# Optimization experiments

Hardware: AMD Instinct MI355X
Metric: run time of the kernel (lower is better)

## Reference

```python
import jax, jax.numpy as jnp
import numpy as np

V, E, H, B, T, O = 50000, 512, 1024, 128, 512, 10


def setup_inputs() -> dict:
    key = jax.random.key(0)
    ks = jax.random.split(key, 12)
    inputs = jax.random.randint(ks[0], (B, T), 0, V)  # token ids
    emb = jax.random.normal(ks[1], (V, E), jnp.float32) * 0.02

    def w(k, shape):
        # stand-in for orthogonal init: scaled gaussian, same shapes/math
        return jax.random.normal(k, shape, jnp.float32) / np.sqrt(shape[0])

    return dict(
        inputs=inputs, emb=emb,
        W_xi=w(ks[2], (E, H)), W_hi=w(ks[3], (H, H)), b_i=jnp.zeros(H, jnp.float32),
        W_xf=w(ks[4], (E, H)), W_hf=w(ks[5], (H, H)), b_f=jnp.ones(H, jnp.float32),
        W_xo=w(ks[6], (E, H)), W_ho=w(ks[7], (H, H)), b_o=jnp.zeros(H, jnp.float32),
        W_xc=w(ks[8], (E, H)), W_hc=w(ks[9], (H, H)), b_c=jnp.zeros(H, jnp.float32),
        W_hq=w(ks[10], (H, O)), b_q=jnp.zeros(O, jnp.float32),
    )


def reference(inputs, emb, W_xi, W_hi, b_i, W_xf, W_hf, b_f,
              W_xo, W_ho, b_o, W_xc, W_hc, b_c, W_hq, b_q):
    x = emb[inputs]  # [B, T, E] embedding lookup
    # Fuse the 4 input projections into one GEMM over the whole sequence
    # (same math as 4 per-step mms: sigmoid/tanh applied per-gate below).
    Wx = jnp.concatenate([W_xi, W_xf, W_xo, W_xc], axis=1)  # [E, 4H]
    Wh = jnp.concatenate([W_hi, W_hf, W_ho, W_hc], axis=1)  # [H, 4H]
    bg = jnp.concatenate([b_i, b_f, b_o, b_c])              # [4H]
    xproj = jnp.einsum('bte,eg->tbg', x, Wx) + bg           # [T, B, 4H]

    hdim = W_hi.shape[0]
    h0 = jnp.zeros((inputs.shape[0], hdim), x.dtype)

    def step(carry, xp):
        h, c = carry
        g = xp + h @ Wh                       # [B, 4H]
        i, f, o, c_tilda = jnp.split(g, 4, axis=-1)
        c = jax.nn.sigmoid(f) * c + jax.nn.sigmoid(i) * jnp.tanh(c_tilda)
        h = jax.nn.sigmoid(o) * jnp.tanh(c)
        return (h, c), None

    (h, _), _ = jax.lax.scan(step, (h0, h0), xproj)
    return jax.nn.softmax(h @ W_hq + b_q, axis=1)  # [B, 10]
```

## Files before the change

kernel.cpp:

```cpp
#include <hip/hip_runtime.h>
#include <hip/hip_fp16.h>

#define V_ 50000
#define E_ 512
#define H_ 1024
#define B_ 128
#define T_ 512
#define NG 4096

typedef _Float16 half8 __attribute__((ext_vector_type(8)));
typedef float f32x4 __attribute__((ext_vector_type(4)));

static constexpr size_t WX_OFF   = 0;
static constexpr size_t WH_OFF   = (size_t)4 << 20;
static constexpr size_t BG_OFF   = (size_t)12 << 20;
static constexpr size_t HBUF_OFF = ((size_t)12 << 20) + ((size_t)64 << 10);
static constexpr size_t BAR_OFF  = ((size_t)12 << 20) + ((size_t)640 << 10);
static constexpr size_t XF_OFF   = (size_t)16 << 20;
static constexpr size_t WS_NEED  = XF_OFF + (size_t)T_ * B_ * E_ * 2;

__device__ __forceinline__ float fsigm(float x) { return 1.f / (1.f + __expf(-x)); }
__device__ __forceinline__ float ftanh(float x) {
  float cx = fminf(fmaxf(x, -15.f), 15.f);
  float e = __expf(2.f * cx);
  return (e - 1.f) / (e + 1.f);
}
__device__ __forceinline__ half8 as_h8(f32x4 x) {
  union { f32x4 f; half8 h; } u; u.f = x; return u.h;
}

__global__ void k_diag(float* __restrict__ out, int n, unsigned wsmb) {
  int i = blockIdx.x * 256 + threadIdx.x;
  if (i < n) out[i] = (i == 0) ? (float)wsmb : 0.1f;
}

__global__ __launch_bounds__(256) void k_prep(
    const float* __restrict__ Wxi, const float* __restrict__ Wxf,
    const float* __restrict__ Wxo, const float* __restrict__ Wxc,
    const float* __restrict__ Whi, const float* __restrict__ Whf,
    const float* __restrict__ Who, const float* __restrict__ Whc,
    const float* __restrict__ bi, const float* __restrict__ bfp,
    const float* __restrict__ bo, const float* __restrict__ bc,
    char* __restrict__ ws) {
  half8* wx = (half8*)(ws + WX_OFF);
  half8* wh = (half8*)(ws + WH_OFF);
  float* bg = (float*)(ws + BG_OFF);
  half8* hb = (half8*)(ws + HBUF_OFF);
  unsigned* bar = (unsigned*)(ws + BAR_OFF);
  const float* WxA[4] = {Wxi, Wxf, Wxo, Wxc};
  const float* WhA[4] = {Whi, Whf, Who, Whc};
  const float* bA[4]  = {bi, bfp, bo, bc};

  const int ZWX = 256 * 16 * 64;
  const int ZWH = 32 * 8 * 32 * 64;
  const int ZBG = NG;
  const int ZHB = 2 * B_ * H_ / 8;
  const int ZBAR = 8 * 128 * 16 + 8 * 64 * 16 + 8 * 32 * 16 + 8 * 16;
  const int total = ZWX + ZWH + ZBG + ZHB + ZBAR;

  for (int it = blockIdx.x * 256 + threadIdx.x; it < total; it += gridDim.x * 256) {
    int i = it;
    if (i < ZWX) {
      int L = i & 63, kt = (i >> 6) & 15, ntg = i >> 10;
      int gate = ntg >> 6;
      int col = ((ntg & 63) << 4) + (L & 15);
      int k0 = (kt << 5) + ((L >> 4) << 3);
      const float* src = WxA[gate] + (size_t)k0 * H_ + col;
      half8 v;
#pragma unroll
      for (int j = 0; j < 8; j++) v[j] = (_Float16)src[(size_t)j * H_];
      wx[i] = v;
    } else if ((i -= ZWX) < ZWH) {
      int L = i & 63, kt = (i >> 6) & 31, nt = (i >> 11) & 7, hbk = i >> 14;
      int ct = nt & 1, g = nt >> 1;
      int col = (hbk << 5) + (ct << 4) + (L & 15);
      int k0 = (kt << 5) + ((L >> 4) << 3);
      const float* src = WhA[g] + (size_t)k0 * H_ + col;
      half8 v;
#pragma unroll
      for (int j = 0; j < 8; j++) v[j] = (_Float16)src[(size_t)j * H_];
      wh[i] = v;
    } else if ((i -= ZWH) < ZBG) {
      bg[i] = bA[i >> 10][i & 1023];
    } else if ((i -= ZBG) < ZHB) {
      half8 z = {};
      hb[i] = z;
    } else {
      i -= ZHB;
      bar[i] = 0u;
    }
  }
}

__global__ __launch_bounds__(256) void k_embed(const int* __restrict__ ids,
                                               const float* __restrict__ emb,
                                               char* __restrict__ ws) {
  half8* xf = (half8*)(ws + XF_OFF);
  const int t = blockIdx.x;
  for (int p = threadIdx.x; p < 128 * 64; p += 256) {
    int b = p >> 6, c8 = p & 63;
    int id = ids[b * T_ + t];
    const float* er = emb + (size_t)id * E_ + (c8 << 3);
    float4 f0 = *(const float4*)er;
    float4 f1 = *(const float4*)(er + 4);
    half8 v;
    v[0] = (_Float16)f0.x; v[1] = (_Float16)f0.y; v[2] = (_Float16)f0.z; v[3] = (_Float16)f0.w;
    v[4] = (_Float16)f1.x; v[5] = (_Float16)f1.y; v[6] = (_Float16)f1.z; v[7] = (_Float16)f1.w;
    int g = b >> 4, row = b & 15;
    xf[((size_t)(t * 8 + g) * 16 + (c8 >> 2)) * 64 + (row | ((c8 & 3) << 4))] = v;
  }
}

__global__ __launch_bounds__(256, 1) void k_lstm(char* __restrict__ ws) {
  __shared__ f32x4 red[4][8][64];
  __shared__ _Float16 hstage2[2][16][16];
  __shared__ unsigned red_ep[4];
  __shared__ int wok[4];
  __shared__ unsigned sslot, sbal;
  const half8* whf = (const half8*)(ws + WH_OFF);
  const half8* wxg = (const half8*)(ws + WX_OFF);
  const float* bgp = (const float*)(ws + BG_OFF);
  _Float16* hbuf = (_Float16*)(ws + HBUF_OFF);
  const half8* xff = (const half8*)(ws + XF_OFF);
  unsigned* bar = (unsigned*)(ws + BAR_OFF);

  const int wg = blockIdx.x;
  const int tid = threadIdx.x;
  const int L = tid & 63, w = tid >> 6;
  const int lo = L & 15, quad = L >> 4;
  unsigned* ctrp = bar + 28672;

  unsigned myxid;
  asm volatile("s_getreg_b32 %0, hwreg(HW_REG_XCC_ID)" : "=s"(myxid));
  myxid &= 7u;
  if (tid == 0)
    sslot = __hip_atomic_fetch_add(&ctrp[myxid * 16], 1u, __ATOMIC_RELAXED,
                                   __HIP_MEMORY_SCOPE_AGENT);
  __syncthreads();
  const unsigned slot = __builtin_amdgcn_readfirstlane(sslot);
  if (tid == 0) {
    unsigned cnt[8];
    while (true) {
      unsigned s = 0;
#pragma unroll
      for (int x = 0; x < 8; x++) {
        cnt[x] = __hip_atomic_load(&ctrp[x * 16], __ATOMIC_RELAXED, __HIP_MEMORY_SCOPE_AGENT);
        s += cnt[x];
      }
      if (s == 256u) break;
      __builtin_amdgcn_s_sleep(4);
    }
    unsigned ok = 1u;
#pragma unroll
    for (int x = 0; x < 8; x++) ok &= (cnt[x] == 32u) ? 1u : 0u;
    sbal = ok;
  }
  __syncthreads();
  const bool balanced = sbal != 0u;
  const int group = balanced ? (int)myxid : (wg & 7);
  const int hblk  = balanced ? (int)slot  : (wg >> 3);
  const int hbase = hblk << 5;
  unsigned* flags = bar + group * 2048;
  unsigned* probe = bar + 16384 + group * 1024;
  unsigned* votes = bar + 24576 + group * 512;

  if (balanced && w < 2 && L == 0) {
    unsigned one = 1u;
    unsigned* pp = &probe[((hblk << 1) + w) << 4];
    asm volatile("global_store_dword %0, %1, off" :: "v"(pp), "v"(one) : "memory");
  }

  half8 bw[8][8];
#pragma unroll
  for (int nt = 0; nt < 8; nt++)
#pragma unroll
    for (int k8 = 0; k8 < 8; k8++)
      bw[nt][k8] = whf[((size_t)(hblk * 8 + nt) * 32 + w * 8 + k8) * 64 + L];
  half8 wxr[8][4];
#pragma unroll
  for (int nt = 0; nt < 8; nt++)
#pragma unroll
    for (int kx = 0; kx < 4; kx++)
      wxr[nt][kx] =
          wxg[(size_t)(((nt >> 1) * 64 + (hblk << 1) + (nt & 1)) * 16 + w * 4 + kx) * 64 + L];

  bool fast = false;
  if (balanced) {
    int okw = 0;
    for (int it = 0; it < 1500 && !okw; ++it) {
      unsigned v = 1u;
      if (L < 16) {
        const unsigned* pp = &probe[(w * 16 + L) << 4];
        unsigned vv;
        asm volatile("global_load_dword %0, %1, off sc0 nt\n\ts_waitcnt vmcnt(0)"
                     : "=v"(vv) : "v"(pp) : "memory");
        v = vv;
      }
      okw = __all((int)(v != 0u));
      if (!okw) __builtin_amdgcn_s_sleep(2);
    }
    if (L == 0) wok[w] = okw;
    __syncthreads();
    const int allok = wok[0] & wok[1] & wok[2] & wok[3];
    if (tid == 0)
      __hip_atomic_store(&votes[hblk << 4], (unsigned)(allok ? 2 : 1),
                         __ATOMIC_RELAXED, __HIP_MEMORY_SCOPE_AGENT);
    unsigned fastu;
    while (true) {
      unsigned v = 2u;
      if (L < 32)
        v = __hip_atomic_load(&votes[L << 4], __ATOMIC_RELAXED, __HIP_MEMORY_SCOPE_AGENT);
      if (__all((int)(v != 0u))) { fastu = (unsigned)__all((int)(v == 2u)); break; }
      __builtin_amdgcn_s_sleep(8);
    }
    fast = fastu != 0;
  }

  const int ct = w & 1, rh = w >> 1;
  float bgr[4] = {};
#pragma unroll
  for (int g = 0; g < 4; g++) bgr[g] = bgp[g * H_ + hbase + (ct << 4) + lo];
  f32x4 cst = {};
  float cst2[2] = {};
  if (tid < 4) red_ep[tid] = 0u;

  half8 ax[4];
  {
    const half8* xb = xff + (size_t)group * (16 * 64);
#pragma unroll
    for (int kx = 0; kx < 4; kx++) ax[kx] = xb[(w * 4 + kx) * 64 + L];
  }
  __syncthreads();

  if (fast) {
    for (int t = 0; t < T_; t++) {
      const _Float16* hb = hbuf + (size_t)(t & 1) * (B_ * H_);
      _Float16* hw = hbuf + (size_t)((t + 1) & 1) * (B_ * H_);

      f32x4 ahf[8];
      const _Float16* hbp =
          hb + (((size_t)group * 32 + (size_t)(w * 8)) << 9) + ((size_t)L << 3);
      const _Float16* hbp2 = hbp + ((size_t)4 << 9);
      asm volatile("global_load_dwordx4 %0, %1, off sc0 nt"             : "=v"(ahf[0]) : "v"(hbp));
      asm volatile("global_load_dwordx4 %0, %1, off offset:1024 sc0 nt" : "=v"(ahf[1]) : "v"(hbp));
      asm volatile("global_load_dwordx4 %0, %1, off offset:2048 sc0 nt" : "=v"(ahf[2]) : "v"(hbp));
      asm volatile("global_load_dwordx4 %0, %1, off offset:3072 sc0 nt" : "=v"(ahf[3]) : "v"(hbp));
      asm volatile("global_load_dwordx4 %0, %1, off sc0 nt"             : "=v"(ahf[4]) : "v"(hbp2));
      asm volatile("global_load_dwordx4 %0, %1, off offset:1024 sc0 nt" : "=v"(ahf[5]) : "v"(hbp2));
      asm volatile("global_load_dwordx4 %0, %1, off offset:2048 sc0 nt" : "=v"(ahf[6]) : "v"(hbp2));
      asm volatile("global_load_dwordx4 %0, %1, off offset:3072 sc0 nt" : "=v"(ahf[7]) : "v"(hbp2));
      asm volatile("s_waitcnt vmcnt(0)" ::: "memory");
      __builtin_amdgcn_sched_barrier(0);

      f32x4 acc[8] = {};
#pragma unroll
      for (int kx = 0; kx < 4; kx++)
#pragma unroll
        for (int nt = 0; nt < 8; nt++)
          acc[nt] = __builtin_amdgcn_mfma_f32_16x16x32_f16(ax[kx], wxr[nt][kx], acc[nt], 0, 0, 0);
#pragma unroll
      for (int k8 = 0; k8 < 8; k8++)
#pragma unroll
        for (int nt = 0; nt < 8; nt++)
          acc[nt] = __builtin_amdgcn_mfma_f32_16x16x32_f16(as_h8(ahf[k8]), bw[nt][k8], acc[nt], 0, 0, 0);
#pragma unroll
      for (int nt = 0; nt < 8; nt++) red[w][nt][L] = acc[nt];
      __syncthreads();

      {
        float ga[4], gb[4];
#pragma unroll
        for (int g = 0; g < 4; g++) {
          f32x4 s = red[0][g * 2 + ct][L];
          s += red[1][g * 2 + ct][L];
          s += red[2][g * 2 + ct][L];
          s += red[3][g * 2 + ct][L];
          ga[g] = rh ? s[2] : s[0];
          gb[g] = rh ? s[3] : s[1];
        }
        if (L == 0)
          __hip_atomic_store(&red_ep[w], (unsigned)(t + 1), __ATOMIC_RELEASE,
                             __HIP_MEMORY_SCOPE_WORKGROUP);
        _Float16* hwb = hw + (((size_t)(group * 32 + hblk)) << 9) + ((size_t)ct << 8) +
                        ((size_t)(lo >> 3) << 7) + ((size_t)quad << 5) + ((size_t)rh << 4) +
                        (size_t)(lo & 7);
#pragma unroll
        for (int rr = 0; rr < 2; rr++) {
          float gi = (rr ? gb[0] : ga[0]) + bgr[0];
          float gf = (rr ? gb[1] : ga[1]) + bgr[1];
          float go = (rr ? gb[2] : ga[2]) + bgr[2];
          float gc = (rr ? gb[3] : ga[3]) + bgr[3];
          float c = fsigm(gf) * cst2[rr] + fsigm(gi) * ftanh(gc);
          cst2[rr] = c;
          union { _Float16 h; unsigned short u; } hv;
          hv.h = (_Float16)(fsigm(go) * ftanh(c));
          unsigned hvu = hv.u;
          asm volatile("global_store_short %0, %1, off"
                       :: "v"(hwb + rr * 8), "v"(hvu) : "memory");
        }
        asm volatile("s_waitcnt vmcnt(0)" ::: "memory");
        unsigned* fptr = &flags[((hblk << 2) + w) << 4];
        unsigned ep = (unsigned)(t + 1);
        if (L == 0)
          asm volatile("global_store_dword %0, %1, off" :: "v"(fptr), "v"(ep) : "memory");
      }

      {
        int tn = (t + 1 < T_) ? (t + 1) : t;
        const half8* xb = xff + ((size_t)tn * 8 + group) * (16 * 64);
#pragma unroll
        for (int kx = 0; kx < 4; kx++) ax[kx] = xb[(w * 4 + kx) * 64 + L];
      }

      if (t + 1 < T_) {
        const unsigned tgt = (unsigned)(t + 1);
        const unsigned* fp32 = &flags[(w * 32 + (L & 31)) << 4];
        while (true) {
          unsigned v = tgt;
          if (L < 32) {
            unsigned vv;
            asm volatile("global_load_dword %0, %1, off sc0 nt\n\ts_waitcnt vmcnt(0)"
                         : "=v"(vv) : "v"(fp32) : "memory");
            v = vv;
          }
          if (__all((int)(v >= tgt))) break;
          __builtin_amdgcn_s_sleep(1);
        }
        while (true) {
          unsigned v = tgt;
          if (L < 4)
            v = __hip_atomic_load(&red_ep[L], __ATOMIC_ACQUIRE, __HIP_MEMORY_SCOPE_WORKGROUP);
          if (__all((int)(v >= tgt))) break;
        }
        __builtin_amdgcn_sched_barrier(0);
      }
    }
  } else {
    for (int t = 0; t < T_; t++) {
      const _Float16* hb = hbuf + (size_t)(t & 1) * (B_ * H_);
      _Float16* hw = hbuf + (size_t)((t + 1) & 1) * (B_ * H_);

      f32x4 ahf[8];
      const _Float16* hbp =
          hb + (((size_t)group * 32 + (size_t)(w * 8)) << 9) + ((size_t)L << 3);
#pragma unroll
      for (int k8 = 0; k8 < 8; k8++) {
        const unsigned long long* ap = (const unsigned long long*)(hbp + ((size_t)k8 << 9));
        union { unsigned long long u[2]; f32x4 f; } cv;
        cv.u[0] = __hip_atomic_load(ap, __ATOMIC_RELAXED, __HIP_MEMORY_SCOPE_AGENT);
        cv.u[1] = __hip_atomic_load(ap + 1, __ATOMIC_RELAXED, __HIP_MEMORY_SCOPE_AGENT);
        ahf[k8] = cv.f;
      }

      f32x4 acc[8] = {};
#pragma unroll
      for (int kx = 0; kx < 4; kx++)
#pragma unroll
        for (int nt = 0; nt < 8; nt++)
          acc[nt] = __builtin_amdgcn_mfma_f32_16x16x32_f16(ax[kx], wxr[nt][kx], acc[nt], 0, 0, 0);
#pragma unroll
      for (int k8 = 0; k8 < 8; k8++)
#pragma unroll
        for (int nt = 0; nt < 8; nt++)
          acc[nt] = __builtin_amdgcn_mfma_f32_16x16x32_f16(as_h8(ahf[k8]), bw[nt][k8], acc[nt], 0, 0, 0);
#pragma unroll
      for (int nt = 0; nt < 8; nt++) red[w][nt][L] = acc[nt];
      __syncthreads();

      if (w < 2) {
        f32x4 gv[4];
#pragma unroll
        for (int g = 0; g < 4; g++) {
          f32x4 s = red[0][g * 2 + w][L];
          s += red[1][g * 2 + w][L];
          s += red[2][g * 2 + w][L];
          s += red[3][g * 2 + w][L];
          gv[g] = s;
        }
        if (L == 0)
          __hip_atomic_store(&red_ep[w], (unsigned)(t + 1), __ATOMIC_RELEASE,
                             __HIP_MEMORY_SCOPE_WORKGROUP);
#pragma unroll
        for (int r = 0; r < 4; r++) {
          float gi = gv[0][r] + bgr[0];
          float gf = gv[1][r] + bgr[1];
          float go = gv[2][r] + bgr[2];
          float gc = gv[3][r] + bgr[3];
          float c = fsigm(gf) * cst[r] + fsigm(gi) * ftanh(gc);
          cst[r] = c;
          hstage2[w][(quad << 2) + r][lo] = (_Float16)(fsigm(go) * ftanh(c));
        }
        __builtin_amdgcn_wave_barrier();
        asm volatile("s_waitcnt lgkmcnt(0)" ::: "memory");
        int rrow = (L >> 1) & 15;
        int cb = ((L >> 5) << 3) + ((L & 1) << 2);
        union { _Float16 h[4]; unsigned long long u; } sv;
#pragma unroll
        for (int q = 0; q < 4; q++) sv.h[q] = hstage2[w][rrow][cb + q];
        unsigned long long* dp =
            (unsigned long long*)(hw + (((size_t)(group * 32 + hblk)) << 9) +
                                  ((size_t)w << 8) + ((size_t)L << 2));
        unsigned* fptr = &flags[((hblk << 1) + w) << 4];
        unsigned ep = (unsigned)(t + 1);
        __hip_atomic_store(dp, sv.u, __ATOMIC_RELAXED, __HIP_MEMORY_SCOPE_AGENT);
        asm volatile("s_waitcnt vmcnt(0)" ::: "memory");
        if (L == 0)
          __hip_atomic_store(fptr, ep, __ATOMIC_RELAXED, __HIP_MEMORY_SCOPE_AGENT);
      }

      {
        int tn = (t + 1 < T_) ? (t + 1) : t;
        const half8* xb = xff + ((size_t)tn * 8 + group) * (16 * 64);
#pragma unroll
        for (int kx = 0; kx < 4; kx++) ax[kx] = xb[(w * 4 + kx) * 64 + L];
      }

      if (t + 1 < T_) {
        const unsigned tgt = (unsigned)(t + 1);
        while (true) {
          unsigned v = tgt;
          if (L < 16)
            v = __hip_atomic_load(&flags[(w * 16 + L) << 4], __ATOMIC_RELAXED,
                                  __HIP_MEMORY_SCOPE_AGENT);
          if (__all((int)(v >= tgt))) break;
          __builtin_amdgcn_s_sleep(1);
        }
        while (true) {
          unsigned v = tgt;
          if (L < 2)
            v = __hip_atomic_load(&red_ep[L], __ATOMIC_ACQUIRE, __HIP_MEMORY_SCOPE_WORKGROUP);
          if (__all((int)(v >= tgt))) break;
        }
        __builtin_amdgcn_sched_barrier(0);
      }
    }
  }
}

__global__ __launch_bounds__(64) void k_final(const char* __restrict__ ws,
                                              const float* __restrict__ Whq,
                                              const float* __restrict__ bq,
                                              float* __restrict__ out) {
  const int b = blockIdx.x;
  const int l = threadIdx.x;
  const _Float16* hf = (const _Float16*)(ws + HBUF_OFF);
  const int g = b >> 4, row = b & 15;
  float s[10];
#pragma unroll
  for (int o = 0; o < 10; o++) s[o] = 0.f;
  for (int k = l; k < H_; k += 64) {
    int kk = k >> 5, q = (k >> 3) & 3, j = k & 7;
    float hv = (float)hf[(((size_t)g * 32 + kk) * 64 + (row | (q << 4))) * 8 + j];
    const float* wr = Whq + (size_t)k * 10;
#pragma unroll
    for (int o = 0; o < 10; o++) s[o] += hv * wr[o];
  }
#pragma unroll
  for (int o = 0; o < 10; o++) {
#pragma unroll
    for (int d = 32; d > 0; d >>= 1) s[o] += __shfl_down(s[o], d);
  }
  if (l == 0) {
    float mx = -1e30f;
    for (int o = 0; o < 10; o++) { s[o] += bq[o]; mx = fmaxf(mx, s[o]); }
    float ssum = 0.f, ex[10];
    for (int o = 0; o < 10; o++) { ex[o] = __expf(s[o] - mx); ssum += ex[o]; }
    for (int o = 0; o < 10; o++) out[b * 10 + o] = ex[o] / ssum;
  }
}

extern "C" void kernel_launch(void* const* d_in, const int* in_sizes, int n_in,
                              void* d_out, int out_size, void* d_ws, size_t ws_size,
                              hipStream_t stream) {
  const int* ids   = (const int*)d_in[0];
  const float* emb = (const float*)d_in[1];
  const float* Wxi = (const float*)d_in[2];
  const float* Whi = (const float*)d_in[3];
  const float* bi  = (const float*)d_in[4];
  const float* Wxf = (const float*)d_in[5];
  const float* Whf = (const float*)d_in[6];
  const float* bfv = (const float*)d_in[7];
  const float* Wxo = (const float*)d_in[8];
  const float* Who = (const float*)d_in[9];
  const float* bo  = (const float*)d_in[10];
  const float* Wxc = (const float*)d_in[11];
  const float* Whc = (const float*)d_in[12];
  const float* bc  = (const float*)d_in[13];
  const float* Whq = (const float*)d_in[14];
  const float* bq  = (const float*)d_in[15];
  float* out = (float*)d_out;
  char* ws = (char*)d_ws;

  if (ws_size < WS_NEED) {
    k_diag<<<(out_size + 255) / 256, 256, 0, stream>>>(out, out_size, (unsigned)(ws_size >> 20));
    return;
  }

  k_prep<<<3217, 256, 0, stream>>>(Wxi, Wxf, Wxo, Wxc, Whi, Whf, Who, Whc, bi, bfv, bo, bc, ws);
  k_embed<<<512, 256, 0, stream>>>(ids, emb, ws);
  k_lstm<<<256, 256, 0, stream>>>(ws);
  k_final<<<128, 64, 0, stream>>>(ws, Whq, bq, out);
}
```

Before: 1.663 ms.

## Replace per-step flag barrier with sentinel-poisoned quad-buffered hidden state polling

Moves the hidden-state buffer from double to quadruple buffering and poisons the buffer two steps ahead with an fp16 infinity sentinel. Consumers poll the hidden-state data itself until no sentinel remains, which removes the separate flag store, the vmcnt drain and the flag spin-wait after each step. The next-step x tile load moves between the two MFMA phases, and the workgroup-local epoch wait moves to just before the reduction writes. The risk is that a real infinity in h would stall the poll, and correctness now depends on store ordering across the wider buffer ring.

```diff
diff --git a/kernel.cpp b/kernel.cpp
--- a/kernel.cpp
+++ b/kernel.cpp
@@ -15,7 +15,7 @@
 static constexpr size_t WH_OFF   = (size_t)4 << 20;
 static constexpr size_t BG_OFF   = (size_t)12 << 20;
 static constexpr size_t HBUF_OFF = ((size_t)12 << 20) + ((size_t)64 << 10);
-static constexpr size_t BAR_OFF  = ((size_t)12 << 20) + ((size_t)640 << 10);
+static constexpr size_t BAR_OFF  = ((size_t)13 << 20) + ((size_t)64 << 10);
 static constexpr size_t XF_OFF   = (size_t)16 << 20;
 static constexpr size_t WS_NEED  = XF_OFF + (size_t)T_ * B_ * E_ * 2;
 
@@ -27,6 +27,9 @@
 }
 __device__ __forceinline__ half8 as_h8(f32x4 x) {
   union { f32x4 f; half8 h; } u; u.f = x; return u.h;
+}
+__device__ __forceinline__ unsigned pkmax(unsigned a, unsigned b) {
+  unsigned r; asm("v_pk_max_f16 %0, %1, %2" : "=v"(r) : "v"(a), "v"(b)); return r;
 }
 
 __global__ void k_diag(float* __restrict__ out, int n, unsigned wsmb) {
@@ -54,9 +57,11 @@
   const int ZWX = 256 * 16 * 64;
   const int ZWH = 32 * 8 * 32 * 64;
   const int ZBG = NG;
-  const int ZHB = 2 * B_ * H_ / 8;
+  const int ZHB = 4 * B_ * H_ / 8;
   const int ZBAR = 8 * 128 * 16 + 8 * 64 * 16 + 8 * 32 * 16 + 8 * 16;
   const int total = ZWX + ZWH + ZBG + ZHB + ZBAR;
+
+  union { unsigned short u; _Float16 h; } sent; sent.u = 0x7C00;
 
   for (int it = blockIdx.x * 256 + threadIdx.x; it < total; it += gridDim.x * 256) {
     int i = it;
@@ -83,8 +88,15 @@
     } else if ((i -= ZWH) < ZBG) {
       bg[i] = bA[i >> 10][i & 1023];
     } else if ((i -= ZBG) < ZHB) {
-      half8 z = {};
-      hb[i] = z;
+      if (i < B_ * H_ / 8) {
+        half8 z = {};
+        hb[i] = z;
+      } else {
+        half8 p;
+#pragma unroll
+        for (int j = 0; j < 8; j++) p[j] = sent.h;
+        hb[i] = p;
+      }
     } else {
       i -= ZHB;
       bar[i] = 0u;
@@ -233,36 +245,90 @@
   __syncthreads();
 
   if (fast) {
+    const unsigned psent = 0x7C00u;
     for (int t = 0; t < T_; t++) {
-      const _Float16* hb = hbuf + (size_t)(t & 1) * (B_ * H_);
-      _Float16* hw = hbuf + (size_t)((t + 1) & 1) * (B_ * H_);
+      const _Float16* hb = hbuf + (size_t)(t & 3) * (B_ * H_);
+      _Float16* hw = hbuf + (size_t)((t + 1) & 3) * (B_ * H_);
+      _Float16* pz = hbuf + (size_t)((t + 2) & 3) * (B_ * H_);
+
+      const size_t upoff = (((size_t)(group * 32 + hblk)) << 9) + ((size_t)ct << 8) +
+                           ((size_t)(lo >> 3) << 7) + ((size_t)quad << 5) +
+                           ((size_t)rh << 4) + (size_t)(lo & 7);
+
+      asm volatile("global_store_short %0, %1, off" :: "v"(pz + upoff), "v"(psent) : "memory");
+      asm volatile("global_store_short %0, %1, off" :: "v"(pz + upoff + 8), "v"(psent) : "memory");
 
       f32x4 ahf[8];
       const _Float16* hbp =
           hb + (((size_t)group * 32 + (size_t)(w * 8)) << 9) + ((size_t)L << 3);
       const _Float16* hbp2 = hbp + ((size_t)4 << 9);
-      asm volatile("global_load_dwordx4 %0, %1, off sc0 nt"             : "=v"(ahf[0]) : "v"(hbp));
-      asm volatile("global_load_dwordx4 %0, %1, off offset:1024 sc0 nt" : "=v"(ahf[1]) : "v"(hbp));
-      asm volatile("global_load_dwordx4 %0, %1, off offset:2048 sc0 nt" : "=v"(ahf[2]) : "v"(hbp));
-      asm volatile("global_load_dwordx4 %0, %1, off offset:3072 sc0 nt" : "=v"(ahf[3]) : "v"(hbp));
-      asm volatile("global_load_dwordx4 %0, %1, off sc0 nt"             : "=v"(ahf[4]) : "v"(hbp2));
-      asm volatile("global_load_dwordx4 %0, %1, off offset:1024 sc0 nt" : "=v"(ahf[5]) : "v"(hbp2));
-      asm volatile("global_load_dwordx4 %0, %1, off offset:2048 sc0 nt" : "=v"(ahf[6]) : "v"(hbp2));
-      asm volatile("global_load_dwordx4 %0, %1, off offset:3072 sc0 nt" : "=v"(ahf[7]) : "v"(hbp2));
+#define AH_LOADS()                                                                              \
+      asm volatile("global_load_dwordx4 %0, %1, off sc0 nt"             : "=v"(ahf[0]) : "v"(hbp));  \
+      asm volatile("global_load_dwordx4 %0, %1, off offset:1024 sc0 nt" : "=v"(ahf[1]) : "v"(hbp));  \
+      asm volatile("global_load_dwordx4 %0, %1, off offset:2048 sc0 nt" : "=v"(ahf[2]) : "v"(hbp));  \
+      asm volatile("global_load_dwordx4 %0, %1, off offset:3072 sc0 nt" : "=v"(ahf[3]) : "v"(hbp));  \
+      asm volatile("global_load_dwordx4 %0, %1, off sc0 nt"             : "=v"(ahf[4]) : "v"(hbp2)); \
+      asm volatile("global_load_dwordx4 %0, %1, off offset:1024 sc0 nt" : "=v"(ahf[5]) : "v"(hbp2)); \
+      asm volatile("global_load_dwordx4 %0, %1, off offset:2048 sc0 nt" : "=v"(ahf[6]) : "v"(hbp2)); \
+      asm volatile("global_load_dwordx4 %0, %1, off offset:3072 sc0 nt" : "=v"(ahf[7]) : "v"(hbp2))
+      AH_LOADS();
       asm volatile("s_waitcnt vmcnt(0)" ::: "memory");
       __builtin_amdgcn_sched_barrier(0);
 
+      {
+#define DW(k, i) __float_as_uint(ahf[k][i])
+        unsigned m0 = DW(0, 0), m1 = DW(0, 1), m2 = DW(0, 2), m3 = DW(0, 3);
+#pragma unroll
+        for (int k8 = 1; k8 < 8; k8++) {
+          m0 = pkmax(m0, DW(k8, 0)); m1 = pkmax(m1, DW(k8, 1));
+          m2 = pkmax(m2, DW(k8, 2)); m3 = pkmax(m3, DW(k8, 3));
+        }
+        unsigned m = pkmax(pkmax(m0, m1), pkmax(m2, m3));
+        int bad = (int)(((m & 0x7FFFu) == 0x7C00u) | (((m >> 16) & 0x7FFFu) == 0x7C00u));
+        while (!__all(!bad)) {
+          __builtin_amdgcn_s_sleep(1);
+          AH_LOADS();
+          asm volatile("s_waitcnt vmcnt(0)" ::: "memory");
+          __builtin_amdgcn_sched_barrier(0);
+          m0 = DW(0, 0); m1 = DW(0, 1); m2 = DW(0, 2); m3 = DW(0, 3);
+#pragma unroll
+          for (int k8 = 1; k8 < 8; k8++) {
+            m0 = pkmax(m0, DW(k8, 0)); m1 = pkmax(m1, DW(k8, 1));
+            m2 = pkmax(m2, DW(k8, 2)); m3 = pkmax(m3, DW(k8, 3));
+          }
+          m = pkmax(pkmax(m0, m1), pkmax(m2, m3));
+          bad = (int)(((m & 0x7FFFu) == 0x7C00u) | (((m >> 16) & 0x7FFFu) == 0x7C00u));
+        }
+#undef DW
+      }
+
       f32x4 acc[8] = {};
 #pragma unroll
       for (int kx = 0; kx < 4; kx++)
 #pragma unroll
         for (int nt = 0; nt < 8; nt++)
           acc[nt] = __builtin_amdgcn_mfma_f32_16x16x32_f16(ax[kx], wxr[nt][kx], acc[nt], 0, 0, 0);
+      {
+        int tn = (t + 1 < T_) ? (t + 1) : t;
+        const half8* xb = xff + ((size_t)tn * 8 + group) * (16 * 64);
+#pragma unroll
+        for (int kx = 0; kx < 4; kx++) ax[kx] = xb[(w * 4 + kx) * 64 + L];
+      }
 #pragma unroll
       for (int k8 = 0; k8 < 8; k8++)
 #pragma unroll
         for (int nt = 0; nt < 8; nt++)
           acc[nt] = __builtin_amdgcn_mfma_f32_16x16x32_f16(as_h8(ahf[k8]), bw[nt][k8], acc[nt], 0, 0, 0);
+
+      if (t > 0) {
+        const unsigned tgt = (unsigned)t;
+        while (true) {
+          unsigned v = tgt;
+          if (L < 4)
+            v = __hip_atomic_load(&red_ep[L], __ATOMIC_ACQUIRE, __HIP_MEMORY_SCOPE_WORKGROUP);
+          if (__all((int)(v >= tgt))) break;
+        }
+      }
 #pragma unroll
       for (int nt = 0; nt < 8; nt++) red[w][nt][L] = acc[nt];
       __syncthreads();
@@ -281,9 +347,7 @@
         if (L == 0)
           __hip_atomic_store(&red_ep[w], (unsigned)(t + 1), __ATOMIC_RELEASE,
                              __HIP_MEMORY_SCOPE_WORKGROUP);
-        _Float16* hwb = hw + (((size_t)(group * 32 + hblk)) << 9) + ((size_t)ct << 8) +
-                        ((size_t)(lo >> 3) << 7) + ((size_t)quad << 5) + ((size_t)rh << 4) +
-                        (size_t)(lo & 7);
+        _Float16* hwb = hw + upoff;
 #pragma unroll
         for (int rr = 0; rr < 2; rr++) {
           float gi = (rr ? gb[0] : ga[0]) + bgr[0];
@@ -298,43 +362,10 @@
           asm volatile("global_store_short %0, %1, off"
                        :: "v"(hwb + rr * 8), "v"(hvu) : "memory");
         }
-        asm volatile("s_waitcnt vmcnt(0)" ::: "memory");
-        unsigned* fptr = &flags[((hblk << 2) + w) << 4];
-        unsigned ep = (unsigned)(t + 1);
-        if (L == 0)
-          asm volatile("global_store_dword %0, %1, off" :: "v"(fptr), "v"(ep) : "memory");
-      }
-
-      {
-        int tn = (t + 1 < T_) ? (t + 1) : t;
-        const half8* xb = xff + ((size_t)tn * 8 + group) * (16 * 64);
-#pragma unroll
-        for (int kx = 0; kx < 4; kx++) ax[kx] = xb[(w * 4 + kx) * 64 + L];
-      }
-
-      if (t + 1 < T_) {
-        const unsigned tgt = (unsigned)(t + 1);
-        const unsigned* fp32 = &flags[(w * 32 + (L & 31)) << 4];
-        while (true) {
-          unsigned v = tgt;
-          if (L < 32) {
-            unsigned vv;
-            asm volatile("global_load_dword %0, %1, off sc0 nt\n\ts_waitcnt vmcnt(0)"
-                         : "=v"(vv) : "v"(fp32) : "memory");
-            v = vv;
-          }
-          if (__all((int)(v >= tgt))) break;
-          __builtin_amdgcn_s_sleep(1);
-        }
-        while (true) {
-          unsigned v = tgt;
-          if (L < 4)
-            v = __hip_atomic_load(&red_ep[L], __ATOMIC_ACQUIRE, __HIP_MEMORY_SCOPE_WORKGROUP);
-          if (__all((int)(v >= tgt))) break;
-        }
-        __builtin_amdgcn_sched_barrier(0);
-      }
+      }
+#undef AH_LOADS
     }
+    asm volatile("s_waitcnt vmcnt(0)" ::: "memory");
   } else {
     for (int t = 0; t < T_; t++) {
       const _Float16* hb = hbuf + (size_t)(t & 1) * (B_ * H_);
```

New measurement: 1.747 ms. 5.1% more time.
